# Kernel optimization log

Measured on AMD Instinct MI355X. Metric: run time of the kernel, lower is better.

Reference implementation:

```python
import jax, jax.numpy as jnp
import numpy as np

B, C, H, W, K = 32, 64, 64, 64, 1024
COMMITMENT_COST = 0.25


def setup_inputs() -> dict:
    key = jax.random.key(0)
    k1, k2, k3, k4 = jax.random.split(key, 4)
    input1 = jax.random.normal(k1, (B, C, H, W), dtype=jnp.float32)
    input2_KL = jax.random.normal(k2, (B,), dtype=jnp.float32)
    x_tilde = jax.random.randint(k3, (B * H * W,), 0, K)  # channel-corrupted indices
    # codebook init: uniform(-1/K, 1/K) as in nn.Embedding init in the module
    weight = jax.random.uniform(k4, (K, C), dtype=jnp.float32, minval=-1.0 / K, maxval=1.0 / K)
    return {"input1": input1, "input2_KL": input2_KL, "weight": weight, "x_tilde": x_tilde}


def reference(input1, input2_KL, weight, x_tilde):
    # [B,C,H,W] -> [B,H,W,C]
    x = jnp.transpose(input1, (0, 2, 3, 1))
    input_shape = x.shape
    flat = x.reshape(-1, weight.shape[1])  # [N, D]
    distances = (jnp.sum(flat * flat, axis=1, keepdims=True)
                 + jnp.sum(weight * weight, axis=1)
                 - 2.0 * jnp.matmul(flat, weight.T))
    idx = jnp.argmin(distances, axis=1)  # [N]
    encodings = jax.nn.one_hot(idx, K, dtype=jnp.float32)  # scatter one-hot
    # channel noise: one_hot(corrupted) - one_hot(clean)
    noise = jax.nn.one_hot(x_tilde, K, dtype=jnp.float32) - encodings
    encodings = encodings + noise
    # recover: [N,K] @ [K,D] -> [N,D]
    quantized = jnp.matmul(encodings, weight).reshape(input_shape)
    e_latent_loss = jnp.mean((jax.lax.stop_gradient(quantized) - x) ** 2)
    q_latent_loss = jnp.mean((quantized - jax.lax.stop_gradient(x)) ** 2)
    loss = q_latent_loss + COMMITMENT_COST * e_latent_loss
    # straight-through estimator
    quantized = x + jax.lax.stop_gradient(quantized - x)
    return loss, input2_KL, jnp.transpose(quantized, (0, 3, 1, 2)), encodings
```

## Files before the change

kernel.cpp:

```cpp
#include <hip/hip_runtime.h>

constexpr int B_ = 32, C_ = 64, H_ = 64, W_ = 64, K_ = 1024;
constexpr int NTOT = B_ * C_ * H_ * W_;
constexpr int NSP  = B_ * H_ * W_;
constexpr int OFF_Q   = 33;
constexpr int OFF_ENC = OFF_Q + NTOT;
constexpr long long ENC_ELEMS = (long long)NSP * K_;
constexpr int ENC_HEAD = 15;
constexpr int ENC_NQ = (int)((ENC_ELEMS - ENC_HEAD - 1) / 4);
constexpr int ENC_BLOCKS = (ENC_NQ + 255) / 256;

constexpr int MAIN_BLOCKS  = NSP / 64;
constexpr int TOTAL_BLOCKS = ENC_BLOCKS + MAIN_BLOCKS;

typedef float v4f __attribute__((ext_vector_type(4)));

__global__ __launch_bounds__(256) void vq_fused(const float* __restrict__ input1,
                                                const int*   __restrict__ x_tilde,
                                                const float* __restrict__ weight,
                                                float* __restrict__ out,
                                                float* __restrict__ ws) {
    const int bid = blockIdx.x;
    if (bid < ENC_BLOCKS) {
        const int b  = bid;
        const int qi = b * 256 + threadIdx.x;
        if (qi >= ENC_NQ) return;
        const int t0 = x_tilde[b];
        const int t1 = x_tilde[(b + 1 < NSP) ? b + 1 : NSP - 1];
        const int col0 = ENC_HEAD + (threadIdx.x << 2);
        v4f v;
        #pragma unroll
        for (int j = 0; j < 4; ++j) {
            const int col = col0 + j;
            ((float*)&v)[j] = (col < 1024) ? ((t0 == col) ? 1.f : 0.f)
                                           : ((t1 == col - 1024) ? 1.f : 0.f);
        }
        *reinterpret_cast<v4f*>(out + OFF_ENC + ENC_HEAD + (qi << 2)) = v;
        return;
    }

    const int mq  = bid - ENC_BLOCKS;
    const int tid = threadIdx.x;
    const int n   = mq * 64 + (tid & 63);
    const int cq  = tid >> 6;
    const int b   = n >> 12;
    const int hw  = n & 4095;
    const int t   = x_tilde[n];
    const float* __restrict__ wrow = weight + (t << 6) + (cq << 4);
    const float* __restrict__ xin  = input1 + (b << 18) + (cq << 16) + hw;
    float* __restrict__ qout = out + OFF_Q + (b << 18) + (cq << 16) + hw;

    const float4 w0 = *reinterpret_cast<const float4*>(wrow);
    const float4 w1 = *reinterpret_cast<const float4*>(wrow + 4);
    const float4 w2 = *reinterpret_cast<const float4*>(wrow + 8);
    const float4 w3 = *reinterpret_cast<const float4*>(wrow + 12);
    const float wv[16] = {w0.x, w0.y, w0.z, w0.w, w1.x, w1.y, w1.z, w1.w,
                          w2.x, w2.y, w2.z, w2.w, w3.x, w3.y, w3.z, w3.w};
    float local = 0.f;
    #pragma unroll
    for (int j = 0; j < 16; ++j) {
        const float x = xin[j << 12];
        const float d = wv[j] - x;
        qout[j << 12] = x + d;
        local += d * d;
    }

    for (int o = 32; o > 0; o >>= 1) local += __shfl_down(local, o);
    __shared__ float sm[4];
    const int lane = tid & 63, wid = tid >> 6;
    if (lane == 0) sm[wid] = local;
    __syncthreads();
    if (tid == 0) {
        ws[mq] = sm[0] + sm[1] + sm[2] + sm[3];
    }
}

__global__ __launch_bounds__(256) void vq_fin(const int* __restrict__ x_tilde,
                                              const float* __restrict__ ws,
                                              const float* __restrict__ kl,
                                              float* __restrict__ out) {
    const int tid = threadIdx.x;
    float local = 0.f;
    #pragma unroll
    for (int k = 0; k < 8; ++k) local += ws[tid + (k << 8)];
    for (int o = 32; o > 0; o >>= 1) local += __shfl_down(local, o);
    __shared__ float sm[4];
    if ((tid & 63) == 0) sm[tid >> 6] = local;
    __syncthreads();
    if (tid == 0) out[0] = 1.25f * (sm[0] + sm[1] + sm[2] + sm[3]) / (float)NTOT;
    if (tid >= 64 && tid < 96) out[1 + tid - 64] = kl[tid - 64];
    if (tid == 96) {
        const int t0 = x_tilde[0];
        #pragma unroll
        for (int j = 0; j < ENC_HEAD; ++j)
            out[OFF_ENC + j] = (t0 == j) ? 1.f : 0.f;
        const int tl = x_tilde[NSP - 1];
        out[OFF_ENC + (int)ENC_ELEMS - 1] = (tl == 1023) ? 1.f : 0.f;
    }
}

extern "C" void kernel_launch(void* const* d_in, const int* in_sizes, int n_in,
                              void* d_out, int out_size, void* d_ws, size_t ws_size,
                              hipStream_t stream) {
    const float* input1 = (const float*)d_in[0];
    const float* kl     = (const float*)d_in[1];
    const float* weight = (const float*)d_in[2];
    const int*   x_til  = (const int*)d_in[3];
    float* out = (float*)d_out;
    float* ws  = (float*)d_ws;

    vq_fused<<<TOTAL_BLOCKS, 256, 0, stream>>>(input1, x_til, weight, out, ws);
    vq_fin<<<1, 256, 0, stream>>>(x_til, ws, kl, out);
}
```

Before: 122.5 us.

## Zero-fill encodings in bulk, then scatter one-hot entries in a second kernel

The first kernel no longer works out each one-hot value from x_tilde. A much smaller set of blocks now zero-fills the whole encodings region with vector stores, each thread issuing 32 stores. The second kernel gets one block per 256 spatial positions, which scatter a single 1.0 into each row, alongside the existing loss-reduction block. The aim is to drop the per-element index loads and compares and the launch overhead of a very large grid on the dominant 512 MB write stream. In exchange it adds a scattered-write pass and depends on ordering across the two kernels for correctness.

```diff
diff --git a/kernel.cpp b/kernel.cpp
--- a/kernel.cpp
+++ b/kernel.cpp
@@ -7,40 +7,40 @@
 constexpr int OFF_ENC = OFF_Q + NTOT;
 constexpr long long ENC_ELEMS = (long long)NSP * K_;
 constexpr int ENC_HEAD = 15;
-constexpr int ENC_NQ = (int)((ENC_ELEMS - ENC_HEAD - 1) / 4);
-constexpr int ENC_BLOCKS = (ENC_NQ + 255) / 256;
+constexpr int ENC_NQ   = (int)((ENC_ELEMS - ENC_HEAD - 1) / 4);
 
-constexpr int MAIN_BLOCKS  = NSP / 64;
-constexpr int TOTAL_BLOCKS = ENC_BLOCKS + MAIN_BLOCKS;
+constexpr int ZB   = 4096;
+constexpr int QPB  = 8192;
+constexpr int MAIN_BLOCKS = NSP / 64;
+constexpr int K1_BLOCKS   = ZB + MAIN_BLOCKS;
 
 typedef float v4f __attribute__((ext_vector_type(4)));
 
-__global__ __launch_bounds__(256) void vq_fused(const float* __restrict__ input1,
-                                                const int*   __restrict__ x_tilde,
-                                                const float* __restrict__ weight,
-                                                float* __restrict__ out,
-                                                float* __restrict__ ws) {
+__global__ __launch_bounds__(256) void vq_k1(const float* __restrict__ input1,
+                                             const int*   __restrict__ x_tilde,
+                                             const float* __restrict__ weight,
+                                             float* __restrict__ out,
+                                             float* __restrict__ ws) {
     const int bid = blockIdx.x;
-    if (bid < ENC_BLOCKS) {
-        const int b  = bid;
-        const int qi = b * 256 + threadIdx.x;
-        if (qi >= ENC_NQ) return;
-        const int t0 = x_tilde[b];
-        const int t1 = x_tilde[(b + 1 < NSP) ? b + 1 : NSP - 1];
-        const int col0 = ENC_HEAD + (threadIdx.x << 2);
-        v4f v;
-        #pragma unroll
-        for (int j = 0; j < 4; ++j) {
-            const int col = col0 + j;
-            ((float*)&v)[j] = (col < 1024) ? ((t0 == col) ? 1.f : 0.f)
-                                           : ((t1 == col - 1024) ? 1.f : 0.f);
+    const int tid = threadIdx.x;
+    if (bid < ZB) {
+        float* p = out + OFF_ENC + ENC_HEAD + bid * (QPB * 4) + (tid << 2);
+        const v4f z = {0.f, 0.f, 0.f, 0.f};
+        if (bid != ZB - 1) {
+            #pragma unroll
+            for (int i = 0; i < 32; ++i)
+                *reinterpret_cast<v4f*>(p + i * 1024) = z;
+        } else {
+            constexpr int LAST_NQ = ENC_NQ - (ZB - 1) * QPB;
+            #pragma unroll
+            for (int i = 0; i < 32; ++i)
+                if (i * 256 + tid < LAST_NQ)
+                    *reinterpret_cast<v4f*>(p + i * 1024) = z;
         }
-        *reinterpret_cast<v4f*>(out + OFF_ENC + ENC_HEAD + (qi << 2)) = v;
         return;
     }
 
-    const int mq  = bid - ENC_BLOCKS;
-    const int tid = threadIdx.x;
+    const int mq  = bid - ZB;
     const int n   = mq * 64 + (tid & 63);
     const int cq  = tid >> 6;
     const int b   = n >> 12;
@@ -75,11 +75,18 @@
     }
 }
 
-__global__ __launch_bounds__(256) void vq_fin(const int* __restrict__ x_tilde,
-                                              const float* __restrict__ ws,
-                                              const float* __restrict__ kl,
-                                              float* __restrict__ out) {
+__global__ __launch_bounds__(256) void vq_k2(const int* __restrict__ x_tilde,
+                                             const float* __restrict__ ws,
+                                             const float* __restrict__ kl,
+                                             float* __restrict__ out) {
+    const int bid = blockIdx.x;
     const int tid = threadIdx.x;
+    if (bid < NSP / 256) {
+        const int n = (bid << 8) + tid;
+        const int t = x_tilde[n];
+        out[OFF_ENC + (n << 10) + t] = 1.0f;
+        return;
+    }
     float local = 0.f;
     #pragma unroll
     for (int k = 0; k < 8; ++k) local += ws[tid + (k << 8)];
@@ -109,6 +116,6 @@
     float* out = (float*)d_out;
     float* ws  = (float*)d_ws;
 
-    vq_fused<<<TOTAL_BLOCKS, 256, 0, stream>>>(input1, x_til, weight, out, ws);
-    vq_fin<<<1, 256, 0, stream>>>(x_til, ws, kl, out);
+    vq_k1<<<K1_BLOCKS, 256, 0, stream>>>(input1, x_til, weight, out, ws);
+    vq_k2<<<NSP / 256 + 1, 256, 0, stream>>>(x_til, ws, kl, out);
 }
```

Measured after the change: 141.4 us. 1.15x slower.
